# Kernel optimization log

Hardware: AMD Instinct MI355X
Metric: run time of the kernel (lower is better)

## Reference

```python
import jax, jax.numpy as jnp
import numpy as np

N = 4096      # num nodes == lr feature dim
H = 8         # heads
HR = 256
C = 2 * HR    # heads * head_dim = 512
D = C // H    # head_dim = 64
EPS = 1e-5


def setup_inputs() -> dict:
    key = jax.random.key(0)
    ks = jax.random.split(key, 10)
    s_in = 1.0 / np.sqrt(N)
    inp = {
        "x": jax.random.normal(ks[0], (N, N), jnp.float32),
        "Wq": jax.random.normal(ks[1], (N, C), jnp.float32) * s_in,
        "bq": jax.random.normal(ks[2], (C,), jnp.float32) * 0.02,
        "Wk": jax.random.normal(ks[3], (N, C), jnp.float32) * s_in,
        "bk": jax.random.normal(ks[4], (C,), jnp.float32) * 0.02,
        "Wv": jax.random.normal(ks[5], (N, C), jnp.float32) * s_in,
        "bv": jax.random.normal(ks[6], (C,), jnp.float32) * 0.02,
        "we": jax.random.normal(ks[7], (C,), jnp.float32),
        "Wskip": jax.random.normal(ks[8], (N, C), jnp.float32) * s_in,
        "bskip": jax.random.normal(ks[9], (C,), jnp.float32) * 0.02,
        "gn_w": jnp.ones((C,), jnp.float32),
        "gn_b": jnp.zeros((C,), jnp.float32),
        "gn_ms": jnp.ones((C,), jnp.float32),
    }
    return inp


def reference(x, Wq, bq, Wk, bk, Wv, bv, we, Wskip, bskip, gn_w, gn_b, gn_ms):
    # TransformerConv on a fully-connected graph; edge (src=j -> tgt=i) attr = x[j, i].
    q = (x @ Wq + bq).reshape(N, H, D)
    k = (x @ Wk + bk).reshape(N, H, D)
    v = (x @ Wv + bv).reshape(N, H, D)
    we_h = we.reshape(H, D)                      # lin_edge weight (no bias)

    xa = x.T                                     # xa[i, j] = edge attr of j -> i
    qk = jnp.einsum('ihd,jhd->ijh', q, k)        # [N, N, H]
    qe = jnp.einsum('ihd,hd->ih', q, we_h)       # [N, H]
    scores = (qk + xa[:, :, None] * qe[:, None, :]) / jnp.sqrt(jnp.float32(D))
    alpha = jax.nn.softmax(scores, axis=1)       # softmax over sources j

    out = jnp.einsum('ijh,jhd->ihd', alpha, v)   # sum_j alpha * value_j
    s = jnp.einsum('ijh,ij->ih', alpha, xa)      # sum_j alpha * edge_attr
    out = out + s[:, :, None] * we_h[None]       # edge embedding added to value too
    out = out.reshape(N, C) + (x @ Wskip + bskip)  # root/skip connection

    # GraphNorm (single graph): per-channel stats over nodes
    mean = out.mean(axis=0)
    centered = out - gn_ms * mean
    var = jnp.mean(centered * centered, axis=0)
    out = gn_w * centered / jnp.sqrt(var + EPS) + gn_b

    # per-node L2 normalization
    out = out / jnp.sqrt(jnp.sum(out * out, axis=1, keepdims=True))
    return out
```

## Files before the change

kernel.cpp:

```cpp
#include <hip/hip_runtime.h>


typedef short s8v __attribute__((ext_vector_type(8)));
typedef unsigned short u16x8 __attribute__((ext_vector_type(8)));
typedef unsigned short u16x4 __attribute__((ext_vector_type(4)));
typedef float f4 __attribute__((ext_vector_type(4)));
typedef unsigned short u16;

__device__ __forceinline__ u16 f2bf(float f) {
    union { float f; unsigned u; } v; v.f = f;
    unsigned r = v.u + 0x7fffu + ((v.u >> 16) & 1u);
    return (u16)(r >> 16);
}
__device__ __forceinline__ float bf2f(u16 h) {
    union { unsigned u; float f; } v; v.u = ((unsigned)h) << 16;
    return v.f;
}

#define GLD16(g, l) __builtin_amdgcn_global_load_lds( \
    (const __attribute__((address_space(1))) void*)(g), \
    (__attribute__((address_space(3))) void*)(l), 16, 0, 0)

__global__ void k_zero(float* stats) { stats[threadIdx.x] = 0.f; }

__global__ __launch_bounds__(256) void k_convx(const float* __restrict__ x,
                                               u16* __restrict__ xb) {
    size_t i = ((size_t)blockIdx.x * 256 + threadIdx.x) * 8;
    float4 a = *(const float4*)(x + i);
    float4 b = *(const float4*)(x + i + 4);
    u16x8 o;
    o[0]=f2bf(a.x); o[1]=f2bf(a.y); o[2]=f2bf(a.z); o[3]=f2bf(a.w);
    o[4]=f2bf(b.x); o[5]=f2bf(b.y); o[6]=f2bf(b.z); o[7]=f2bf(b.w);
    *(u16x8*)(xb + i) = o;
}

__global__ __launch_bounds__(256) void k_transw(const float* __restrict__ Wq,
                                                const float* __restrict__ Wk,
                                                const float* __restrict__ Wv,
                                                const float* __restrict__ Ws,
                                                u16* __restrict__ wb) {
    __shared__ float tile[64][65];
    int k0 = blockIdx.x * 64;
    int n0 = blockIdx.y * 64;
    const float* W = (n0 < 512) ? Wq : (n0 < 1024) ? Wk : (n0 < 1536) ? Wv : Ws;
    int col0 = n0 & 511;
    int t = threadIdx.x;
#pragma unroll
    for (int q = 0; q < 4; q++) {
        int idx = t + 256 * q;
        int row = idx >> 4, c4 = (idx & 15) * 4;
        float4 v = *(const float4*)&W[(size_t)(k0 + row) * 512 + col0 + c4];
        tile[row][c4 + 0] = v.x; tile[row][c4 + 1] = v.y;
        tile[row][c4 + 2] = v.z; tile[row][c4 + 3] = v.w;
    }
    __syncthreads();
#pragma unroll
    for (int q = 0; q < 2; q++) {
        int idx = t + 256 * q;
        int row = idx >> 3, c8 = (idx & 7) * 8;
        u16x8 o;
#pragma unroll
        for (int j = 0; j < 8; j++) o[j] = f2bf(tile[c8 + j][row]);
        *(u16x8*)&wb[(size_t)(n0 + row) * 4096 + k0 + c8] = o;
    }
}

__global__ __launch_bounds__(256) void k_gemm(const u16* __restrict__ xb,
                                              const u16* __restrict__ wb,
                                              const float* __restrict__ bq,
                                              const float* __restrict__ bk,
                                              const float* __restrict__ bv,
                                              const float* __restrict__ bs,
                                              u16* __restrict__ qkvs) {
    __shared__ __align__(16) u16 A_lds[128 * 32];
    __shared__ __align__(16) u16 B_lds[128 * 32];
    int tid = threadIdx.x;
    int w = tid >> 6, lane = tid & 63;
    int wr = w >> 1, wc = w & 1;
    int m0 = blockIdx.y * 128, n0 = blockIdx.x * 128;

    const f4 fz = {0.f, 0.f, 0.f, 0.f};
    f4 acc[4][4];
#pragma unroll
    for (int r = 0; r < 4; r++)
#pragma unroll
        for (int t = 0; t < 4; t++) acc[r][t] = fz;

    int srow = lane >> 2;
    int scol = (lane & 3) * 8;
    const u16* gA0 = xb + (size_t)(m0 + 32 * w + srow) * 4096 + scol;
    const u16* gB0 = wb + (size_t)(n0 + 32 * w + srow) * 4096 + scol;

    for (int kt = 0; kt < 128; ++kt) {
        int k0 = kt * 32;
        GLD16(gA0 + k0,             &A_lds[(32 * w) * 32]);
        GLD16(gA0 + k0 + 16 * 4096, &A_lds[(32 * w + 16) * 32]);
        GLD16(gB0 + k0,             &B_lds[(32 * w) * 32]);
        GLD16(gB0 + k0 + 16 * 4096, &B_lds[(32 * w + 16) * 32]);
        __syncthreads();
        s8v a[4], b[4];
#pragma unroll
        for (int r = 0; r < 4; r++)
            a[r] = *(const s8v*)&A_lds[(wr * 64 + 16 * r + (lane & 15)) * 32 + (lane >> 4) * 8];
#pragma unroll
        for (int t = 0; t < 4; t++)
            b[t] = *(const s8v*)&B_lds[(wc * 64 + 16 * t + (lane & 15)) * 32 + (lane >> 4) * 8];
#pragma unroll
        for (int r = 0; r < 4; r++)
#pragma unroll
            for (int t = 0; t < 4; t++)
                acc[r][t] = __builtin_amdgcn_mfma_f32_16x16x32_bf16(a[r], b[t], acc[r][t], 0, 0, 0);
        __syncthreads();
    }

#pragma unroll
    for (int t = 0; t < 4; t++) {
        int n = n0 + wc * 64 + 16 * t + (lane & 15);
        int seg = n >> 9, o = n & 511;
        const float* bp = (seg == 0) ? bq : (seg == 1) ? bk : (seg == 2) ? bv : bs;
        float bias = bp[o];
#pragma unroll
        for (int r = 0; r < 4; r++) {
            int mbase = m0 + wr * 64 + 16 * r + ((lane >> 4) << 2);
#pragma unroll
            for (int q2 = 0; q2 < 4; q2++)
                qkvs[(size_t)(mbase + q2) * 2048 + n] = f2bf(acc[r][t][q2] + bias);
        }
    }
}

__global__ __launch_bounds__(256) void k_transv(const u16* __restrict__ qkvs,
                                                u16* __restrict__ vt) {
    __shared__ unsigned tile[64 * 65];
    int j0 = blockIdx.x * 64, d0 = blockIdx.y * 64;
    int t = threadIdx.x;
#pragma unroll
    for (int q = 0; q < 2; q++) {
        int idx = t + 256 * q;
        int row = idx >> 3, c8 = (idx & 7) * 8;
        s8v v = *(const s8v*)&qkvs[(size_t)(j0 + row) * 2048 + 1024 + d0 + c8];
#pragma unroll
        for (int j = 0; j < 8; j++) tile[row * 65 + c8 + j] = (unsigned)(u16)v[j];
    }
    __syncthreads();
#pragma unroll
    for (int q = 0; q < 2; q++) {
        int idx = t + 256 * q;
        int row = idx >> 3, c8 = (idx & 7) * 8;
        u16x8 o;
#pragma unroll
        for (int j = 0; j < 8; j++) o[j] = (u16)tile[(c8 + j) * 65 + row];
        *(u16x8*)&vt[(size_t)(d0 + row) * 4096 + j0 + c8] = o;
    }
}

__global__ __launch_bounds__(256, 4) void k_attn(const u16* __restrict__ qkvs,
                                                 const u16* __restrict__ xb,
                                                 const u16* __restrict__ vt,
                                                 const float* __restrict__ we,
                                                 float* __restrict__ o_part,
                                                 float* __restrict__ lsa_part) {
    __shared__ __align__(16) u16 K_lds[64 * 64];
    __shared__ __align__(16) u16 V_lds[64 * 64];
    __shared__ __align__(16) u16 P_lds[64 * 72];
    __shared__ __align__(16) u16 X_lds[64 * 72];
    __shared__ float qe8[64];

    int tid = threadIdx.x;
    int w = tid >> 6, lane = tid & 63;
    int L = lane & 15, q = lane >> 4;
    int i0 = blockIdx.x * 64;
    int h = blockIdx.y, hc = h * 64;
    int sp = blockIdx.z;

    int r8 = lane >> 3;
    int csw = ((lane & 7) ^ r8) * 8;

    {
        const u16* g0 = qkvs + (size_t)i0 * 2048 + hc;
#pragma unroll
        for (int ih = 0; ih < 2; ih++) {
            int rb = 16 * w + 8 * ih;
            GLD16(g0 + (size_t)(rb + r8) * 2048 + csw, &K_lds[rb * 64]);
        }
    }
    __syncthreads();

    s8v qf[2];
#pragma unroll
    for (int c = 0; c < 2; c++) {
        int row = 16 * w + L;
        qf[c] = *(const s8v*)&K_lds[row * 64 + (((4 * c + q) ^ (row & 7)) * 8)];
    }
    if (tid < 64) {
        float s = 0.f;
        int r7 = tid & 7;
#pragma unroll
        for (int d = 0; d < 64; d++)
            s += bf2f(K_lds[tid * 64 + ((d >> 3) ^ r7) * 8 + (d & 7)]) * we[hc + d];
        qe8[tid] = s * 0.125f;
    }
    __syncthreads();

    float qe_r[4];
#pragma unroll
    for (int r = 0; r < 4; r++) qe_r[r] = qe8[16 * w + 4 * q + r];

    const f4 fz = {0.f, 0.f, 0.f, 0.f};
    f4 o_acc[4];
    float l_p[4], sa_p[4];
#pragma unroll
    for (int r = 0; r < 4; r++) { l_p[r] = 0.f; sa_p[r] = 0.f; }
#pragma unroll
    for (int t = 0; t < 4; t++) o_acc[t] = fz;

    for (int jt64 = 0; jt64 < 32; ++jt64) {
        int j0 = sp * 2048 + jt64 * 64;
        {
            const u16* g0 = qkvs + (size_t)j0 * 2048 + 512 + hc;
#pragma unroll
            for (int ih = 0; ih < 2; ih++) {
                int rb = 16 * w + 8 * ih;
                GLD16(g0 + (size_t)(rb + r8) * 2048 + csw, &K_lds[rb * 64]);
            }
        }
        {
            const u16* g0 = vt + (size_t)hc * 4096 + j0;
#pragma unroll
            for (int ih = 0; ih < 2; ih++) {
                int rb = 16 * w + 8 * ih;
                GLD16(g0 + (size_t)(rb + r8) * 4096 + csw, &V_lds[rb * 64]);
            }
        }
#pragma unroll
        for (int qq = 0; qq < 2; qq++) {
            int idx = tid + 256 * qq;
            int row = idx >> 3, c8 = (idx & 7) * 8;
            *(s8v*)&X_lds[row * 72 + c8] =
                *(const s8v*)&xb[(size_t)(j0 + row) * 4096 + i0 + c8];
        }
        __syncthreads();

#pragma unroll
        for (int jt = 0; jt < 4; jt++) {
            int n = L + 16 * jt;
            int n7 = n & 7;
            s8v b0 = *(const s8v*)&K_lds[n * 64 + ((q ^ n7) * 8)];
            s8v b1 = *(const s8v*)&K_lds[n * 64 + (((4 + q) ^ n7) * 8)];
            f4 acc = fz;
            acc = __builtin_amdgcn_mfma_f32_16x16x32_bf16(qf[0], b0, acc, 0, 0, 0);
            acc = __builtin_amdgcn_mfma_f32_16x16x32_bf16(qf[1], b1, acc, 0, 0, 0);
            u16x4 xv4 = *(const u16x4*)&X_lds[n * 72 + 16 * w + 4 * q];
#pragma unroll
            for (int r = 0; r < 4; r++) {
                float xx = bf2f(xv4[r]);
                float s = fminf(acc[r] * 0.125f + xx * qe_r[r], 80.f);
                float p = __expf(s);
                l_p[r] += p;
                sa_p[r] += p * xx;
                P_lds[(16 * w + 4 * q + r) * 72 + n] = f2bf(p);
            }
        }

        {
            int row = 16 * w + L;
            s8v a0 = *(const s8v*)&P_lds[row * 72 + q * 8];
            s8v a1 = *(const s8v*)&P_lds[row * 72 + 32 + q * 8];
#pragma unroll
            for (int t = 0; t < 4; t++) {
                int n = L + 16 * t;
                int n7 = n & 7;
                s8v b0 = *(const s8v*)&V_lds[n * 64 + ((q ^ n7) * 8)];
                s8v b1 = *(const s8v*)&V_lds[n * 64 + (((4 + q) ^ n7) * 8)];
                o_acc[t] = __builtin_amdgcn_mfma_f32_16x16x32_bf16(a0, b0, o_acc[t], 0, 0, 0);
                o_acc[t] = __builtin_amdgcn_mfma_f32_16x16x32_bf16(a1, b1, o_acc[t], 0, 0, 0);
            }
        }
        __syncthreads();
    }

#pragma unroll
    for (int r = 0; r < 4; r++) {
        float l = l_p[r], sa = sa_p[r];
        l += __shfl_xor(l, 1);  sa += __shfl_xor(sa, 1);
        l += __shfl_xor(l, 2);  sa += __shfl_xor(sa, 2);
        l += __shfl_xor(l, 4);  sa += __shfl_xor(sa, 4);
        l += __shfl_xor(l, 8);  sa += __shfl_xor(sa, 8);
        int i = i0 + 16 * w + 4 * q + r;
#pragma unroll
        for (int t = 0; t < 4; t++)
            o_part[((size_t)sp * 4096 + i) * 512 + hc + L + 16 * t] = o_acc[t][r];
        if (L == 0) {
            size_t bi = (((size_t)sp * 4096 + i) * 8 + h) * 2;
            lsa_part[bi] = l;
            lsa_part[bi + 1] = sa;
        }
    }
}

__global__ __launch_bounds__(512) void k_comb(const float* __restrict__ o_part,
                                              const float* __restrict__ lsa,
                                              const u16* __restrict__ qkvs,
                                              const float* __restrict__ we,
                                              float* __restrict__ out_pre,
                                              float* __restrict__ stats) {
    int c = threadIdx.x;
    int r0 = blockIdx.x * 64;
    int h = c >> 6;
    float wec = we[c];
    float s = 0.f, s2 = 0.f;
    for (int ii = 0; ii < 64; ii++) {
        int i = r0 + ii;
        size_t b0 = ((size_t)i * 8 + h) * 2;
        size_t b1 = (((size_t)4096 + i) * 8 + h) * 2;
        float l = lsa[b0] + lsa[b1];
        float sa = lsa[b0 + 1] + lsa[b1 + 1];
        float o = o_part[(size_t)i * 512 + c] + o_part[((size_t)4096 + i) * 512 + c];
        float inv = 1.f / l;
        float v = (o + sa * wec) * inv + bf2f(qkvs[(size_t)i * 2048 + 1536 + c]);
        out_pre[(size_t)i * 512 + c] = v;
        s += v; s2 += v * v;
    }
    atomicAdd(&stats[c], s);
    atomicAdd(&stats[512 + c], s2);
}

__global__ __launch_bounds__(512) void k_final(const float* __restrict__ out_pre,
                                               const float* __restrict__ stats,
                                               const float* __restrict__ gn_w,
                                               const float* __restrict__ gn_b,
                                               const float* __restrict__ gn_ms,
                                               float* __restrict__ out) {
    __shared__ float red[8];
    int c = threadIdx.x;
    int i = blockIdx.x;
    float mean = stats[c] * (1.f / 4096.f);
    float ex2 = stats[512 + c] * (1.f / 4096.f);
    float g = gn_ms[c];
    float var = ex2 - (2.f * g - g * g) * mean * mean;
    float y = gn_w[c] * (out_pre[(size_t)i * 512 + c] - g * mean) * rsqrtf(var + 1e-5f) + gn_b[c];
    float qv = y * y;
    qv += __shfl_xor(qv, 1);  qv += __shfl_xor(qv, 2);  qv += __shfl_xor(qv, 4);
    qv += __shfl_xor(qv, 8);  qv += __shfl_xor(qv, 16); qv += __shfl_xor(qv, 32);
    if ((c & 63) == 0) red[c >> 6] = qv;
    __syncthreads();
    float tot = 0.f;
#pragma unroll
    for (int k = 0; k < 8; k++) tot += red[k];
    out[(size_t)i * 512 + c] = y * rsqrtf(tot);
}

extern "C" void kernel_launch(void* const* d_in, const int* in_sizes, int n_in,
                              void* d_out, int out_size, void* d_ws, size_t ws_size,
                              hipStream_t stream) {
    (void)in_sizes; (void)n_in; (void)out_size; (void)ws_size;
    const float* x    = (const float*)d_in[0];
    const float* Wq   = (const float*)d_in[1];
    const float* bq   = (const float*)d_in[2];
    const float* Wk   = (const float*)d_in[3];
    const float* bk   = (const float*)d_in[4];
    const float* Wv   = (const float*)d_in[5];
    const float* bv   = (const float*)d_in[6];
    const float* we   = (const float*)d_in[7];
    const float* Ws   = (const float*)d_in[8];
    const float* bs   = (const float*)d_in[9];
    const float* gnw  = (const float*)d_in[10];
    const float* gnb  = (const float*)d_in[11];
    const float* gnms = (const float*)d_in[12];
    float* out = (float*)d_out;

    char* ws = (char*)d_ws;
    u16* xb        = (u16*)(ws);
    float* out_pre = (float*)(ws);
    u16* wb        = (u16*)(ws + (size_t)33554432);
    float* o_part  = (float*)(ws + (size_t)33554432);
    u16* qkvs      = (u16*)(ws + (size_t)50331648);
    u16* vt        = (u16*)(ws + (size_t)67108864);
    float* lsa     = (float*)(ws + (size_t)71303168);
    float* stats   = (float*)(ws + (size_t)71303168 + 524288);

    k_zero<<<1, 1024, 0, stream>>>(stats);
    k_convx<<<8192, 256, 0, stream>>>(x, xb);
    k_transw<<<dim3(64, 32), 256, 0, stream>>>(Wq, Wk, Wv, Ws, wb);
    k_gemm<<<dim3(16, 32), 256, 0, stream>>>(xb, wb, bq, bk, bv, bs, qkvs);
    k_transv<<<dim3(64, 8), 256, 0, stream>>>(qkvs, vt);
    k_attn<<<dim3(64, 8, 2), 256, 0, stream>>>(qkvs, xb, vt, we, o_part, lsa);
    k_comb<<<64, 512, 0, stream>>>(o_part, lsa, qkvs, we, out_pre, stats);
    k_final<<<4096, 512, 0, stream>>>(out_pre, stats, gnw, gnb, gnms, out);
}
```

Before: 344.5 us.

## Fuse V transpose and stats zeroing into producers, fold softmax scale into Q

```diff
diff --git a/kernel.cpp b/kernel.cpp
--- a/kernel.cpp
+++ b/kernel.cpp
@@ -12,6 +12,10 @@
     unsigned r = v.u + 0x7fffu + ((v.u >> 16) & 1u);
     return (u16)(r >> 16);
 }
+__device__ __forceinline__ u16 f2bf_hu(float f) {
+    union { float f; unsigned u; } v; v.f = f;
+    return (u16)((v.u + 0x8000u) >> 16);
+}
 __device__ __forceinline__ float bf2f(u16 h) {
     union { unsigned u; float f; } v; v.u = ((unsigned)h) << 16;
     return v.f;
@@ -21,10 +25,13 @@
     (const __attribute__((address_space(1))) void*)(g), \
     (__attribute__((address_space(3))) void*)(l), 16, 0, 0)
 
-__global__ void k_zero(float* stats) { stats[threadIdx.x] = 0.f; }
-
 __global__ __launch_bounds__(256) void k_convx(const float* __restrict__ x,
-                                               u16* __restrict__ xb) {
+                                               u16* __restrict__ xb,
+                                               float* __restrict__ stats) {
+    if (blockIdx.x == 0) {
+        int t = threadIdx.x;
+        stats[t] = 0.f; stats[256 + t] = 0.f; stats[512 + t] = 0.f; stats[768 + t] = 0.f;
+    }
     size_t i = ((size_t)blockIdx.x * 256 + threadIdx.x) * 8;
     float4 a = *(const float4*)(x + i);
     float4 b = *(const float4*)(x + i + 4);
@@ -71,7 +78,8 @@
                                               const float* __restrict__ bk,
                                               const float* __restrict__ bv,
                                               const float* __restrict__ bs,
-                                              u16* __restrict__ qkvs) {
+                                              u16* __restrict__ qkvs,
+                                              u16* __restrict__ vt) {
     __shared__ __align__(16) u16 A_lds[128 * 32];
     __shared__ __align__(16) u16 B_lds[128 * 32];
     int tid = threadIdx.x;
@@ -119,38 +127,20 @@
         int seg = n >> 9, o = n & 511;
         const float* bp = (seg == 0) ? bq : (seg == 1) ? bk : (seg == 2) ? bv : bs;
         float bias = bp[o];
+        float scale = (seg == 0) ? 0.1803368801f : 1.f;
 #pragma unroll
         for (int r = 0; r < 4; r++) {
             int mbase = m0 + wr * 64 + 16 * r + ((lane >> 4) << 2);
-#pragma unroll
-            for (int q2 = 0; q2 < 4; q2++)
-                qkvs[(size_t)(mbase + q2) * 2048 + n] = f2bf(acc[r][t][q2] + bias);
-        }
-    }
-}
-
-__global__ __launch_bounds__(256) void k_transv(const u16* __restrict__ qkvs,
-                                                u16* __restrict__ vt) {
-    __shared__ unsigned tile[64 * 65];
-    int j0 = blockIdx.x * 64, d0 = blockIdx.y * 64;
-    int t = threadIdx.x;
-#pragma unroll
-    for (int q = 0; q < 2; q++) {
-        int idx = t + 256 * q;
-        int row = idx >> 3, c8 = (idx & 7) * 8;
-        s8v v = *(const s8v*)&qkvs[(size_t)(j0 + row) * 2048 + 1024 + d0 + c8];
-#pragma unroll
-        for (int j = 0; j < 8; j++) tile[row * 65 + c8 + j] = (unsigned)(u16)v[j];
-    }
-    __syncthreads();
-#pragma unroll
-    for (int q = 0; q < 2; q++) {
-        int idx = t + 256 * q;
-        int row = idx >> 3, c8 = (idx & 7) * 8;
-        u16x8 o;
-#pragma unroll
-        for (int j = 0; j < 8; j++) o[j] = (u16)tile[(c8 + j) * 65 + row];
-        *(u16x8*)&vt[(size_t)(d0 + row) * 4096 + j0 + c8] = o;
+            u16x4 hv;
+#pragma unroll
+            for (int q2 = 0; q2 < 4; q2++) {
+                u16 h = f2bf((acc[r][t][q2] + bias) * scale);
+                hv[q2] = h;
+                qkvs[(size_t)(mbase + q2) * 2048 + n] = h;
+            }
+            if (seg == 2)
+                *(u16x4*)&vt[(size_t)(n - 1024) * 4096 + mbase] = hv;
+        }
     }
 }
 
@@ -198,7 +188,7 @@
 #pragma unroll
         for (int d = 0; d < 64; d++)
             s += bf2f(K_lds[tid * 64 + ((d >> 3) ^ r7) * 8 + (d & 7)]) * we[hc + d];
-        qe8[tid] = s * 0.125f;
+        qe8[tid] = s;
     }
     __syncthreads();
 
@@ -254,11 +244,11 @@
 #pragma unroll
             for (int r = 0; r < 4; r++) {
                 float xx = bf2f(xv4[r]);
-                float s = fminf(acc[r] * 0.125f + xx * qe_r[r], 80.f);
-                float p = __expf(s);
+                float s = fminf(acc[r] + xx * qe_r[r], 115.f);
+                float p = __builtin_amdgcn_exp2f(s);
                 l_p[r] += p;
                 sa_p[r] += p * xx;
-                P_lds[(16 * w + 4 * q + r) * 72 + n] = f2bf(p);
+                P_lds[(16 * w + 4 * q + r) * 72 + n] = f2bf_hu(p);
             }
         }
 
@@ -379,11 +369,9 @@
     float* lsa     = (float*)(ws + (size_t)71303168);
     float* stats   = (float*)(ws + (size_t)71303168 + 524288);
 
-    k_zero<<<1, 1024, 0, stream>>>(stats);
-    k_convx<<<8192, 256, 0, stream>>>(x, xb);
+    k_convx<<<8192, 256, 0, stream>>>(x, xb, stats);
     k_transw<<<dim3(64, 32), 256, 0, stream>>>(Wq, Wk, Wv, Ws, wb);
-    k_gemm<<<dim3(16, 32), 256, 0, stream>>>(xb, wb, bq, bk, bv, bs, qkvs);
-    k_transv<<<dim3(64, 8), 256, 0, stream>>>(qkvs, vt);
+    k_gemm<<<dim3(16, 32), 256, 0, stream>>>(xb, wb, bq, bk, bv, bs, qkvs, vt);
     k_attn<<<dim3(64, 8, 2), 256, 0, stream>>>(qkvs, xb, vt, we, o_part, lsa);
     k_comb<<<64, 512, 0, stream>>>(o_part, lsa, qkvs, we, out_pre, stats);
     k_final<<<4096, 512, 0, stream>>>(out_pre, stats, gnw, gnb, gnms, out);
```

Result: faster. 337.3 us (-2.1%).
